# Kernel optimization log

Hardware: AMD Instinct MI355X
Metric: run time of the kernel (lower is better)

## Reference

```python
import jax, jax.numpy as jnp
import numpy as np

B, H, W, CIN, COUT, KH, KW = 16, 64, 64, 256, 256, 3, 3


def setup_inputs() -> dict:
    key = jax.random.key(0)
    k1, k2, k3 = jax.random.split(key, 3)
    x = jax.random.normal(k1, (B, H, W, CIN), dtype=jnp.float32)
    style = jax.random.normal(k2, (B, CIN), dtype=jnp.float32)
    # glorot-ish scale for the base kernel
    kernel = jax.random.normal(k3, (KH, KW, CIN, COUT), dtype=jnp.float32) * 0.05
    return {"x": x, "style": style, "kernel": kernel}


def reference(x, style, kernel):
    b = x.shape[0]
    cout = kernel.shape[-1]
    # Modulate: per-sample weights [B, kh, kw, Cin, Cout]
    w = kernel[None] * (style[:, None, None, :, None] + 1.0)
    # Demodulate: L2 normalize over (kh, kw, Cin) per (sample, out-channel)
    w = w / jnp.sqrt(jnp.sum(jnp.square(w), axis=(1, 2, 3), keepdims=True) + 1e-8)
    # Batch-as-groups grouped conv: x -> [1, B*Cin, H, W]
    xg = jnp.transpose(x, (0, 3, 1, 2)).reshape(1, -1, x.shape[1], x.shape[2])
    # w -> [kh, kw, Cin, B*Cout]
    wg = jnp.transpose(w, (1, 2, 3, 0, 4)).reshape(w.shape[1], w.shape[2], w.shape[3], -1)
    y = jax.lax.conv_general_dilated(
        xg, wg,
        window_strides=(1, 1),
        padding='SAME',
        dimension_numbers=('NCHW', 'HWIO', 'NCHW'),
        feature_group_count=b,
    )
    # [1, B*Cout, H, W] -> [B, H, W, Cout]
    y = y.reshape(b, cout, y.shape[2], y.shape[3])
    return jnp.transpose(y, (0, 2, 3, 1))
```

## Files before the change

### kernel.cpp

```cpp
#include <hip/hip_runtime.h>


#define HH 64
#define WW 64
#define CI 256
#define CO 256
#define XP 66
#define CIPITCH 40
#define XCOLS 66

typedef float    f32x4 __attribute__((ext_vector_type(4)));
typedef _Float16 f16x8 __attribute__((ext_vector_type(8)));
typedef __fp16   fp16x2 __attribute__((ext_vector_type(2)));

__device__ __forceinline__ unsigned pk2(float a, float b) {
    fp16x2 h = __builtin_amdgcn_cvt_pkrtz(a, b);
    return __builtin_bit_cast(unsigned, h);
}

__global__ __launch_bounds__(256) void prep(
    const float* __restrict__ kern,
    const float* __restrict__ style,
    ushort* __restrict__ Wt2,
    float* __restrict__ scale2)
{
    __shared__ ushort tile[64][65];
    __shared__ float  sqt[64][65];
    __shared__ float  st2l[16][64];

    const int kt = blockIdx.x >> 2;
    const int ct = blockIdx.x & 3;
    const int k0 = kt * 64, c0 = ct * 64;
    const int ci0 = k0 & 255;
    const int tid = threadIdx.x;
    const int r = tid >> 2, q = tid & 3;

    #pragma unroll
    for (int p = 0; p < 4; ++p) {
        const int i = p * 256 + tid;
        const int bb = i >> 6, rr = i & 63;
        const float s = style[bb * CI + ci0 + rr] + 1.0f;
        st2l[bb][rr] = s * s;
    }

    const float* src = kern + (size_t)(k0 + r) * CO + c0 + q * 16;
    #pragma unroll
    for (int j = 0; j < 16; ++j) {
        const float v = src[j];
        _Float16 h = (_Float16)v;
        tile[q * 16 + j][r] = __builtin_bit_cast(unsigned short, h);
        sqt[r][q * 16 + j] = v * v;
    }
    __syncthreads();

    const int co_w = c0 + r;
    #pragma unroll
    for (int j = 0; j < 16; ++j) {
        const int k   = k0 + q * 16 + j;
        const int t9  = k >> 8;
        const int rem = k & 255;
        const int cc  = rem >> 5;
        const int fq  = (rem >> 3) & 3;
        const int e   = k & 7;
        Wt2[((((size_t)cc * 9 + t9) * 4 + fq) * 256 + co_w) * 8 + e] =
            tile[r][q * 16 + j];
    }

    const int co = tid & 63;
    const int bq = tid >> 6;
    float acc[4] = {0.f, 0.f, 0.f, 0.f};
    #pragma unroll 4
    for (int rr = 0; rr < 64; ++rr) {
        const float s = sqt[rr][co];
        #pragma unroll
        for (int bb = 0; bb < 4; ++bb)
            acc[bb] += s * st2l[bq * 4 + bb][rr];
    }
    #pragma unroll
    for (int bb = 0; bb < 4; ++bb)
        atomicAdd(&scale2[(bq * 4 + bb) * CO + c0 + co], acc[bb]);
}

__global__ __launch_bounds__(256) void xmod_k(
    const float* __restrict__ x,
    const float* __restrict__ style,
    ushort* __restrict__ Xm)
{
    const int b  = blockIdx.x / XP;
    const int hh = blockIdx.x - b * XP;
    const int tid = threadIdx.x;
    ushort* dst = Xm + ((size_t)(b * XP + hh)) * XP * CI;

    if (hh == 0 || hh == XP - 1) {
        const uint4 z = {0, 0, 0, 0};
        #pragma unroll
        for (int p = 0; p < 9; ++p) {
            const int t = p * 256 + tid;
            if (t < 2112) *(uint4*)(dst + t * 8) = z;
        }
        return;
    }

    const int l = tid & 63;
    const int q = tid >> 6;
    const int ci0 = l * 4;
    const int rg = hh - 1;

    f32x4 st = *(const f32x4*)(style + b * CI + ci0);
    st.x += 1.f; st.y += 1.f; st.z += 1.f; st.w += 1.f;

    const float* srow = x + ((size_t)(b * HH + rg)) * WW * CI + ci0;
    #pragma unroll
    for (int k = 0; k < 17; ++k) {
        const int cc = q + 4 * k;
        if (cc < XP) {
            uint2 u = {0, 0};
            if (cc >= 1 && cc <= WW) {
                const f32x4 v = *(const f32x4*)(srow + (size_t)(cc - 1) * CI);
                const f32x4 m = v * st;
                u.x = pk2(m.x, m.y);
                u.y = pk2(m.z, m.w);
            }
            *(uint2*)(dst + cc * CI + ci0) = u;
        }
    }
}

__global__ __launch_bounds__(256) void gemm_dma(
    const ushort* __restrict__ Xm,
    const ushort* __restrict__ Wt2,
    const float* __restrict__ scale2,
    float* __restrict__ y)
{
    __shared__ __align__(16) ushort xs2[2][10240];
    __shared__ __align__(16) ushort bs[3 * 4096];

    const int tid  = threadIdx.x;
    const int lane = tid & 63;
    const int wave = tid >> 6;

    const int mtile = blockIdx.x >> 1;
    const int n0    = (blockIdx.x & 1) * 128;
    const int p0    = mtile * 128;
    const int b     = p0 >> 12;
    const int h0    = (p0 >> 6) & 63;

    const int wm = (wave & 1) * 64;
    const int wn = (wave >> 1) * 64;
    const int fr = lane & 15;
    const int fq = lane >> 4;

    const ushort* xb = Xm + (size_t)b * XP * XP * CI;

    int xoff5[5];
    #pragma unroll
    for (int p = 0; p < 5; ++p) {
        const int task = p * 256 + tid;
        const int rc = task >> 2;
        const int ch = task & 3;
        xoff5[p] = (rc < 264)
            ? (((h0 + rc / 66) * XP + (rc % 66)) * CI + ch * 8)
            : 0;
    }

    auto issue_xs = [&](int cn, int bufn) {
        #pragma unroll
        for (int p = 0; p < 5; ++p) {
            const ushort* g = xb + xoff5[p] + cn * 32;
            const ushort* l = &xs2[bufn][(p * 256 + (tid & ~63)) * 8];
            __builtin_amdgcn_global_load_lds(
                (const __attribute__((address_space(1))) void*)g,
                (__attribute__((address_space(3))) void*)l,
                16, 0, 0);
        }
    };

    auto issue_tile = [&](int cn, int t9n, int bufn) {
        const ushort* gb = Wt2 + ((size_t)((cn * 9 + t9n) * 4) * 256 + n0) * 8;
        #pragma unroll
        for (int p = 0; p < 2; ++p) {
            const int task = p * 256 + tid;
            const ushort* g = gb + (size_t)(((task >> 7) << 8) + (task & 127)) * 8;
            const ushort* l = bs + bufn * 4096 + (p * 256 + (tid & ~63)) * 8;
            __builtin_amdgcn_global_load_lds(
                (const __attribute__((address_space(1))) void*)g,
                (__attribute__((address_space(3))) void*)l,
                16, 0, 0);
        }
    };

    f32x4 acc[4][4] = {};

    issue_xs(0, 0);
    issue_tile(0, 0, 0);
    issue_tile(0, 1, 1);

    for (int c = 0; c < 8; ++c) {
        const int xbuf = c & 1;
        #pragma unroll
        for (int t9 = 0; t9 < 9; ++t9) {
            if ((t9 == 5 || t9 == 6) && c < 7)
                asm volatile("s_waitcnt vmcnt(7) lgkmcnt(0)" ::: "memory");
            else
                asm volatile("s_waitcnt vmcnt(2) lgkmcnt(0)" ::: "memory");
            __builtin_amdgcn_s_barrier();

            {
                const int t2 = (t9 + 2 >= 9) ? t9 - 7 : t9 + 2;
                const int c2 = (t9 >= 7) ? c + 1 : c;
                if (c2 < 8) issue_tile(c2, t2, t2 % 3);
            }
            if (t9 == 4 && c < 7) issue_xs(c + 1, xbuf ^ 1);

            const int dh  = t9 / 3;
            const int dw  = t9 - dh * 3;
            const int buf = t9 % 3;

            f16x8 af[4], bf[4];
            #pragma unroll
            for (int i = 0; i < 4; ++i) {
                const int mb = wm + i * 16;
                const int rc = ((mb >> 6) + dh) * XCOLS + (mb & 63) + fr + dw;
                af[i] = *(const f16x8*)(&xs2[xbuf][rc * 32 + fq * 8]);
            }
            #pragma unroll
            for (int j = 0; j < 4; ++j)
                bf[j] = *(const f16x8*)(bs + buf * 4096 + fq * 1024
                                        + (wn + j * 16 + fr) * 8);
            #pragma unroll
            for (int i = 0; i < 4; ++i)
                #pragma unroll
                for (int j = 0; j < 4; ++j)
                    acc[i][j] = __builtin_amdgcn_mfma_f32_16x16x32_f16(
                        af[i], bf[j], acc[i][j], 0, 0, 0);
        }
    }

    float sc[4];
    #pragma unroll
    for (int j = 0; j < 4; ++j)
        sc[j] = __frsqrt_rn(scale2[b * CO + n0 + wn + j * 16 + fr] + 1e-8f);
    #pragma unroll
    for (int i = 0; i < 4; ++i) {
        const int m_base = p0 + wm + i * 16 + fq * 4;
        #pragma unroll
        for (int j = 0; j < 4; ++j) {
            float* yp = y + (size_t)m_base * CO + n0 + wn + j * 16 + fr;
            #pragma unroll
            for (int r = 0; r < 4; ++r)
                yp[(size_t)r * CO] = acc[i][j][r] * sc[j];
        }
    }
}

__global__ __launch_bounds__(256) void gemm_lds(
    const float* __restrict__ x,
    const ushort* __restrict__ Wt2,
    const float* __restrict__ style,
    const float* __restrict__ scale2,
    float* __restrict__ y)
{
    __shared__ __align__(16) ushort xs[4 * XCOLS * CIPITCH];
    __shared__ __align__(16) ushort bs[3 * 4096];
    __shared__ float s_style[CI];

    const int tid  = threadIdx.x;
    const int lane = tid & 63;
    const int wave = tid >> 6;

    const int mtile = blockIdx.x >> 1;
    const int n0    = (blockIdx.x & 1) * 128;
    const int p0    = mtile * 128;
    const int b     = p0 >> 12;
    const int h0    = (p0 >> 6) & 63;

    s_style[tid] = style[b * CI + tid] + 1.0f;

    const int wm = (wave & 1) * 64;
    const int wn = (wave >> 1) * 64;
    const int fr = lane & 15;
    const int fq = lane >> 4;
    const int xlane = fr * CIPITCH + fq * 8;

    auto issue_tile = [&](int cn, int t9n, int bufn) {
        const ushort* gb = Wt2 + ((size_t)((cn * 9 + t9n) * 4) * 256 + n0) * 8;
        #pragma unroll
        for (int p = 0; p < 2; ++p) {
            const int task = p * 256 + tid;
            const ushort* g = gb + (size_t)(((task >> 7) << 8) + (task & 127)) * 8;
            const ushort* l = bs + bufn * 4096 + (p * 256 + (tid & ~63)) * 8;
            __builtin_amdgcn_global_load_lds(
                (const __attribute__((address_space(1))) void*)g,
                (__attribute__((address_space(3))) void*)l,
                16, 0, 0);
        }
    };

    f32x4 acc[4][4] = {};

    issue_tile(0, 0, 0);
    issue_tile(0, 1, 1);

    for (int c = 0; c < 8; ++c) {
        #pragma unroll
        for (int t9 = 0; t9 < 9; ++t9) {
            asm volatile("s_waitcnt vmcnt(2) lgkmcnt(0)" ::: "memory");
            __builtin_amdgcn_s_barrier();

            if (t9 == 0) {
                #pragma unroll
                for (int p = 0; p < 9; ++p) {
                    const int task = p * 256 + tid;
                    if (task < 2112) {
                        const int rowcol = task >> 3;
                        const int chunk  = task & 7;
                        const int row = rowcol / XCOLS;
                        const int col = rowcol - row * XCOLS;
                        const int rg = h0 - 1 + row;
                        const int cg = col - 1;
                        f32x4 v = {0.f, 0.f, 0.f, 0.f};
                        if ((unsigned)rg < 64u && (unsigned)cg < 64u)
                            v = *(const f32x4*)(x + ((size_t)((b * HH + rg) * WW + cg)) * CI
                                                  + c * 32 + chunk * 4);
                        const f32x4 st = *(const f32x4*)(s_style + c * 32 + chunk * 4);
                        const f32x4 m = v * st;
                        uint2 u;
                        u.x = pk2(m.x, m.y);
                        u.y = pk2(m.z, m.w);
                        *(uint2*)(xs + rowcol * CIPITCH + chunk * 4) = u;
                    }
                }
                asm volatile("s_waitcnt lgkmcnt(0)" ::: "memory");
                __builtin_amdgcn_s_barrier();
            }

            {
                const int t2 = (t9 + 2 >= 9) ? t9 - 7 : t9 + 2;
                const int c2 = (t9 >= 7) ? c + 1 : c;
                if (c2 < 8) issue_tile(c2, t2, t2 % 3);
            }

            const int buf = t9 % 3;
            const int dh  = t9 / 3;
            const int dw  = t9 - dh * 3;

            f16x8 af[4], bf[4];
            #pragma unroll
            for (int i = 0; i < 4; ++i) {
                const int mb   = wm + i * 16;
                const int mrow = (mb >> 6) + dh;
                const int mcol = (mb & 63) + dw;
                af[i] = *(const f16x8*)(xs + (mrow * XCOLS + mcol) * CIPITCH + xlane);
            }
            #pragma unroll
            for (int j = 0; j < 4; ++j)
                bf[j] = *(const f16x8*)(bs + buf * 4096 + fq * 1024
                                        + (wn + j * 16 + fr) * 8);
            #pragma unroll
            for (int i = 0; i < 4; ++i)
                #pragma unroll
                for (int j = 0; j < 4; ++j)
                    acc[i][j] = __builtin_amdgcn_mfma_f32_16x16x32_f16(
                        af[i], bf[j], acc[i][j], 0, 0, 0);
        }
    }

    float sc[4];
    #pragma unroll
    for (int j = 0; j < 4; ++j)
        sc[j] = __frsqrt_rn(scale2[b * CO + n0 + wn + j * 16 + fr] + 1e-8f);
    #pragma unroll
    for (int i = 0; i < 4; ++i) {
        const int m_base = p0 + wm + i * 16 + fq * 4;
        #pragma unroll
        for (int j = 0; j < 4; ++j) {
            float* yp = y + (size_t)m_base * CO + n0 + wn + j * 16 + fr;
            #pragma unroll
            for (int r = 0; r < 4; ++r)
                yp[(size_t)r * CO] = acc[i][j][r] * sc[j];
        }
    }
}

extern "C" void kernel_launch(void* const* d_in, const int* in_sizes, int n_in,
                              void* d_out, int out_size, void* d_ws, size_t ws_size,
                              hipStream_t stream) {
    const float* x     = (const float*)d_in[0];
    const float* style = (const float*)d_in[1];
    const float* kern  = (const float*)d_in[2];
    float* out = (float*)d_out;

    float*  scale2 = (float*)d_ws;
    ushort* Wt2    = (ushort*)((char*)d_ws + 16384);

    const size_t xm_off  = 16384 + 1179648;
    const size_t xm_size = (size_t)16 * XP * XP * CI * 2;

    hipMemsetAsync(scale2, 0, 16 * CO * sizeof(float), stream);
    prep<<<144, 256, 0, stream>>>(kern, style, Wt2, scale2);

    if (ws_size >= xm_off + xm_size) {
        ushort* Xm = (ushort*)((char*)d_ws + xm_off);
        xmod_k<<<16 * XP, 256, 0, stream>>>(x, style, Xm);
        gemm_dma<<<512 * 2, 256, 0, stream>>>(Xm, Wt2, scale2, out);
    } else {
        gemm_lds<<<512 * 2, 256, 0, stream>>>(x, Wt2, style, scale2, out);
    }
}
```

Measured before the change: 248.0 us.

## Single-buffer activation tile with XOR swizzle to fit three blocks per CU

Replaces the double-buffered activation LDS tile with a single buffer, cutting LDS per block so launch_bounds(256,3) can fit three workgroups per CU. The next channel chunk's activations now load only after the last tap's fragments are read, behind an extra barrier. An XOR swizzle on the 16-byte chunk index is added to reduce LDS bank conflicts on fragment reads, and s_setprio is raised around the MFMA block. The trade-off is less intra-block prefetch overlap, which now relies on other resident blocks to hide load latency, plus possible register pressure from the occupancy bound.

Result: faster. 209.0 us (-15.7%).

```diff
diff --git a/kernel.cpp b/kernel.cpp
--- a/kernel.cpp
+++ b/kernel.cpp
@@ -126,13 +126,13 @@
     }
 }
 
-__global__ __launch_bounds__(256) void gemm_dma(
+__global__ __launch_bounds__(256, 3) void gemm_dma(
     const ushort* __restrict__ Xm,
     const ushort* __restrict__ Wt2,
     const float* __restrict__ scale2,
     float* __restrict__ y)
 {
-    __shared__ __align__(16) ushort xs2[2][10240];
+    __shared__ __align__(16) ushort xs[10240];
     __shared__ __align__(16) ushort bs[3 * 4096];
 
     const int tid  = threadIdx.x;
@@ -152,22 +152,17 @@
 
     const ushort* xb = Xm + (size_t)b * XP * XP * CI;
 
-    int xoff5[5];
-    #pragma unroll
-    for (int p = 0; p < 5; ++p) {
-        const int task = p * 256 + tid;
-        const int rc = task >> 2;
-        const int ch = task & 3;
-        xoff5[p] = (rc < 264)
-            ? (((h0 + rc / 66) * XP + (rc % 66)) * CI + ch * 8)
-            : 0;
-    }
-
-    auto issue_xs = [&](int cn, int bufn) {
+    auto issue_xs = [&](int cn) {
         #pragma unroll
         for (int p = 0; p < 5; ++p) {
-            const ushort* g = xb + xoff5[p] + cn * 32;
-            const ushort* l = &xs2[bufn][(p * 256 + (tid & ~63)) * 8];
+            const int task = p * 256 + tid;
+            const int rc = task >> 2;
+            const int ch = (task & 3) ^ ((rc >> 1) & 3);
+            const int off = (rc < 264)
+                ? (((h0 + rc / 66) * XP + (rc % 66)) * CI + ch * 8 + cn * 32)
+                : 0;
+            const ushort* g = xb + off;
+            const ushort* l = xs + (p * 256 + (tid & ~63)) * 8;
             __builtin_amdgcn_global_load_lds(
                 (const __attribute__((address_space(1))) void*)g,
                 (__attribute__((address_space(3))) void*)l,
@@ -191,48 +186,74 @@
 
     f32x4 acc[4][4] = {};
 
-    issue_xs(0, 0);
+    issue_xs(0);
     issue_tile(0, 0, 0);
     issue_tile(0, 1, 1);
 
     for (int c = 0; c < 8; ++c) {
-        const int xbuf = c & 1;
         #pragma unroll
         for (int t9 = 0; t9 < 9; ++t9) {
-            if ((t9 == 5 || t9 == 6) && c < 7)
-                asm volatile("s_waitcnt vmcnt(7) lgkmcnt(0)" ::: "memory");
+            if (c == 7 && t9 == 8)
+                asm volatile("s_waitcnt vmcnt(0) lgkmcnt(0)" ::: "memory");
             else
                 asm volatile("s_waitcnt vmcnt(2) lgkmcnt(0)" ::: "memory");
             __builtin_amdgcn_s_barrier();
 
-            {
+            const int dh  = t9 / 3;
+            const int dw  = t9 - dh * 3;
+            const int buf = t9 % 3;
+
+            if (t9 < 8) {
                 const int t2 = (t9 + 2 >= 9) ? t9 - 7 : t9 + 2;
                 const int c2 = (t9 >= 7) ? c + 1 : c;
                 if (c2 < 8) issue_tile(c2, t2, t2 % 3);
+
+                f16x8 af[4], bf[4];
+                #pragma unroll
+                for (int i = 0; i < 4; ++i) {
+                    const int mb = wm + i * 16;
+                    const int rc = ((mb >> 6) + dh) * XCOLS + (mb & 63) + fr + dw;
+                    af[i] = *(const f16x8*)(xs + rc * 32 + ((fq ^ ((rc >> 1) & 3)) * 8));
+                }
+                #pragma unroll
+                for (int j = 0; j < 4; ++j)
+                    bf[j] = *(const f16x8*)(bs + buf * 4096 + fq * 1024
+                                            + (wn + j * 16 + fr) * 8);
+                __builtin_amdgcn_s_setprio(1);
+                #pragma unroll
+                for (int i = 0; i < 4; ++i)
+                    #pragma unroll
+                    for (int j = 0; j < 4; ++j)
+                        acc[i][j] = __builtin_amdgcn_mfma_f32_16x16x32_f16(
+                            af[i], bf[j], acc[i][j], 0, 0, 0);
+                __builtin_amdgcn_s_setprio(0);
+            } else {
+                f16x8 af[4], bf[4];
+                #pragma unroll
+                for (int i = 0; i < 4; ++i) {
+                    const int mb = wm + i * 16;
+                    const int rc = ((mb >> 6) + dh) * XCOLS + (mb & 63) + fr + dw;
+                    af[i] = *(const f16x8*)(xs + rc * 32 + ((fq ^ ((rc >> 1) & 3)) * 8));
+                }
+                #pragma unroll
+                for (int j = 0; j < 4; ++j)
+                    bf[j] = *(const f16x8*)(bs + buf * 4096 + fq * 1024
+                                            + (wn + j * 16 + fr) * 8);
+                if (c < 7) {
+                    asm volatile("s_waitcnt lgkmcnt(0)" ::: "memory");
+                    __builtin_amdgcn_s_barrier();
+                    issue_xs(c + 1);
+                    issue_tile(c + 1, 1, 1);
+                }
+                __builtin_amdgcn_s_setprio(1);
+                #pragma unroll
+                for (int i = 0; i < 4; ++i)
+                    #pragma unroll
+                    for (int j = 0; j < 4; ++j)
+                        acc[i][j] = __builtin_amdgcn_mfma_f32_16x16x32_f16(
+                            af[i], bf[j], acc[i][j], 0, 0, 0);
+                __builtin_amdgcn_s_setprio(0);
             }
-            if (t9 == 4 && c < 7) issue_xs(c + 1, xbuf ^ 1);
-
-            const int dh  = t9 / 3;
-            const int dw  = t9 - dh * 3;
-            const int buf = t9 % 3;
-
-            f16x8 af[4], bf[4];
-            #pragma unroll
-            for (int i = 0; i < 4; ++i) {
-                const int mb = wm + i * 16;
-                const int rc = ((mb >> 6) + dh) * XCOLS + (mb & 63) + fr + dw;
-                af[i] = *(const f16x8*)(&xs2[xbuf][rc * 32 + fq * 8]);
-            }
-            #pragma unroll
-            for (int j = 0; j < 4; ++j)
-                bf[j] = *(const f16x8*)(bs + buf * 4096 + fq * 1024
-                                        + (wn + j * 16 + fr) * 8);
-            #pragma unroll
-            for (int i = 0; i < 4; ++i)
-                #pragma unroll
-                for (int j = 0; j < 4; ++j)
-                    acc[i][j] = __builtin_amdgcn_mfma_f32_16x16x32_f16(
-                        af[i], bf[j], acc[i][j], 0, 0, 0);
         }
     }
 
@@ -260,7 +281,7 @@
     const float* __restrict__ scale2,
     float* __restrict__ y)
 {
-    __shared__ __align__(16) ushort xs[4 * XCOLS * CIPITCH];
+    __shared__ __align__(16) ushort xsf[4 * XCOLS * CIPITCH];
     __shared__ __align__(16) ushort bs[3 * 4096];
     __shared__ float s_style[CI];
 
@@ -327,7 +348,7 @@
                         uint2 u;
                         u.x = pk2(m.x, m.y);
                         u.y = pk2(m.z, m.w);
-                        *(uint2*)(xs + rowcol * CIPITCH + chunk * 4) = u;
+                        *(uint2*)(xsf + rowcol * CIPITCH + chunk * 4) = u;
                     }
                 }
                 asm volatile("s_waitcnt lgkmcnt(0)" ::: "memory");
@@ -350,7 +371,7 @@
                 const int mb   = wm + i * 16;
                 const int mrow = (mb >> 6) + dh;
                 const int mcol = (mb & 63) + dw;
-                af[i] = *(const f16x8*)(xs + (mrow * XCOLS + mcol) * CIPITCH + xlane);
+                af[i] = *(const f16x8*)(xsf + (mrow * XCOLS + mcol) * CIPITCH + xlane);
             }
             #pragma unroll
             for (int j = 0; j < 4; ++j)
```
